# Performance work log

Hardware: AMD Instinct MI355X
Metric: run time of the kernel (lower is better)

The kernel has to match this reference:

```python
import jax, jax.numpy as jnp
import numpy as np

N_NODES = 50000
N_EDGES = 1600000
IN_DIM = 128
HEADS = 8
OUT_C = 16  # per-head channels; HEADS*OUT_C == IN_DIM -> residual active
NEG_SLOPE = 0.2
BN_EPS = 1e-5


def setup_inputs() -> dict:
    key = jax.random.key(0)
    ks = jax.random.split(key, 8)
    x = jax.random.normal(ks[0], (N_NODES, IN_DIM), dtype=jnp.float32)
    edge_index = jax.random.randint(ks[1], (2, N_EDGES), 0, N_NODES, dtype=jnp.int64)
    # GATConv params (PyG: shared lin for src/dst on single-tensor input)
    W = jax.random.normal(ks[2], (IN_DIM, HEADS * OUT_C), dtype=jnp.float32) / np.sqrt(IN_DIM)
    att_src = jax.random.normal(ks[3], (HEADS, OUT_C), dtype=jnp.float32) / np.sqrt(OUT_C)
    att_dst = jax.random.normal(ks[4], (HEADS, OUT_C), dtype=jnp.float32) / np.sqrt(OUT_C)
    bias = jnp.zeros((HEADS * OUT_C,), dtype=jnp.float32)
    # BatchNorm1d affine params
    gamma = jnp.ones((HEADS * OUT_C,), dtype=jnp.float32)
    beta = jnp.zeros((HEADS * OUT_C,), dtype=jnp.float32)
    return {"x": x, "edge_index": edge_index, "W": W, "att_src": att_src,
            "att_dst": att_dst, "bias": bias, "gamma": gamma, "beta": beta}


def reference(x, edge_index, W, att_src, att_dst, bias, gamma, beta):
    N = x.shape[0]
    H, C = att_src.shape
    src, dst = edge_index[0], edge_index[1]

    xl = (x @ W).reshape(N, H, C)                      # [N,H,C]
    a_src = jnp.sum(xl * att_src[None], axis=-1)       # [N,H]
    a_dst = jnp.sum(xl * att_dst[None], axis=-1)       # [N,H]

    e = jax.nn.leaky_relu(a_src[src] + a_dst[dst], NEG_SLOPE)  # [E,H]
    # segment softmax over incoming edges of each dst node
    m = jax.ops.segment_max(e, dst, num_segments=N)    # [N,H], -inf for empty
    m = jnp.where(jnp.isfinite(m), m, 0.0)
    ex = jnp.exp(e - m[dst])                           # [E,H]
    denom = jax.ops.segment_sum(ex, dst, num_segments=N)
    alpha = ex / (denom[dst] + 1e-16)                  # [E,H]

    out = jax.ops.segment_sum(alpha[:, :, None] * xl[src], dst, num_segments=N)  # [N,H,C]
    h = out.reshape(N, H * C) + bias

    # BatchNorm1d (training mode: batch statistics, biased variance)
    mean = jnp.mean(h, axis=0)
    var = jnp.mean((h - mean) ** 2, axis=0)
    h = (h - mean) * jax.lax.rsqrt(var + BN_EPS) * gamma + beta

    h = jax.nn.relu(h)
    return x + h  # residual (in_dim == H*C)
```

## Files before the change

### kernel.cpp

```cpp
#include <hip/hip_runtime.h>
#include <hip/hip_fp16.h>
#include <math.h>

#define N_NODES 50000
#define N_EDGES 1600000
#define DIM 128
#define HEADS 8
#define NEG_SLOPE 0.2f
#define BN_EPS 1e-5f

typedef _Float16 f16x8 __attribute__((ext_vector_type(8)));
typedef float f32x4 __attribute__((ext_vector_type(4)));

__global__ void k_wprep(const float* __restrict__ W, __half* __restrict__ Wh,
                        int* __restrict__ bcur, float* __restrict__ gsums) {
    const int t = threadIdx.x;
    if (blockIdx.x == 0 && t < 256) bcur[t] = 0;
    if (blockIdx.x == 1 && t < 256) gsums[t] = 0.f;
    const int tid = blockIdx.x * 256 + t;
    const int g = tid >> 6;
    const int lane = tid & 63;
    const int nt = g >> 2, kt = g & 3;
    const int q = lane >> 4, n = lane & 15;
    #pragma unroll
    for (int j = 0; j < 8; ++j)
        Wh[(size_t)(g * 64 + lane) * 8 + j] =
            __float2half(W[(kt * 32 + q * 8 + j) * DIM + nt * 16 + n]);
}

__global__ __launch_bounds__(256) void k_lin(const float* __restrict__ x,
                      const __half* __restrict__ Wh, const float* __restrict__ att_s,
                      const float* __restrict__ att_d, __half* __restrict__ xlh,
                      float* __restrict__ a_src, float* __restrict__ a_dst) {
    const int wave = threadIdx.x >> 6;
    const int lane = threadIdx.x & 63;
    const int q = lane >> 4, n = lane & 15;
    const int nb = (blockIdx.x * 4 + wave) * 16;

    const int rowA = min(nb + n, N_NODES - 1);
    const float* xr = x + (size_t)rowA * DIM;
    f16x8 a[4];
    #pragma unroll
    for (int kt = 0; kt < 4; ++kt) {
        const float4 p0 = *(const float4*)(xr + kt * 32 + q * 8);
        const float4 p1 = *(const float4*)(xr + kt * 32 + q * 8 + 4);
        a[kt][0] = (_Float16)p0.x; a[kt][1] = (_Float16)p0.y;
        a[kt][2] = (_Float16)p0.z; a[kt][3] = (_Float16)p0.w;
        a[kt][4] = (_Float16)p1.x; a[kt][5] = (_Float16)p1.y;
        a[kt][6] = (_Float16)p1.z; a[kt][7] = (_Float16)p1.w;
    }

    f32x4 acc[8];
    #pragma unroll
    for (int nt = 0; nt < 8; ++nt) acc[nt] = (f32x4){0.f, 0.f, 0.f, 0.f};

    const f16x8* wb = (const f16x8*)Wh;
    #pragma unroll
    for (int nt = 0; nt < 8; ++nt) {
        #pragma unroll
        for (int kt = 0; kt < 4; ++kt) {
            const f16x8 b = wb[(nt * 4 + kt) * 64 + lane];
            acc[nt] = __builtin_amdgcn_mfma_f32_16x16x32_f16(a[kt], b, acc[nt], 0, 0, 0);
        }
    }

    const int r0 = nb + q * 4;
    #pragma unroll
    for (int nt = 0; nt < 8; ++nt) {
        const float as = att_s[nt * 16 + n];
        const float ad = att_d[nt * 16 + n];
        #pragma unroll
        for (int r = 0; r < 4; ++r) {
            const int row = r0 + r;
            const float v = acc[nt][r];
            float s = v * as;
            float d = v * ad;
            #pragma unroll
            for (int off = 8; off; off >>= 1) {
                s += __shfl_xor(s, off, 16);
                d += __shfl_xor(d, off, 16);
            }
            if (row < N_NODES) {
                xlh[(size_t)row * DIM + nt * 16 + n] = __float2half(v);
                if (n == 0) {
                    a_src[row * HEADS + nt] = s;
                    a_dst[row * HEADS + nt] = d;
                }
            }
        }
    }
}

#define NBUCK 196
#define SEGCAP 12288
#define CHUNK 8192
#define NB_A ((N_EDGES + CHUNK - 1) / CHUNK)

__global__ __launch_bounds__(1024) void k_binA(const int* __restrict__ ei,
                                               int* __restrict__ bcur,
                                               unsigned int* __restrict__ pairs) {
    __shared__ int hist[NBUCK], excl[NBUCK], gbase[NBUCK], cnt2[NBUCK];
    __shared__ int sc[256];
    __shared__ unsigned int buf[CHUNK];
    const int t = threadIdx.x;
    const int base = blockIdx.x * CHUNK;
    const int cnt = min(CHUNK, N_EDGES - base);

    for (int j = t; j < NBUCK; j += 1024) { hist[j] = 0; cnt2[j] = 0; }
    __syncthreads();
    for (int i = t * 4; i < cnt; i += 4096) {
        const int4 dv = *(const int4*)(ei + N_EDGES + base + i);
        atomicAdd(&hist[dv.x >> 8], 1);
        atomicAdd(&hist[dv.y >> 8], 1);
        atomicAdd(&hist[dv.z >> 8], 1);
        atomicAdd(&hist[dv.w >> 8], 1);
    }
    __syncthreads();
    if (t < 256) sc[t] = (t < NBUCK) ? hist[t] : 0;
    __syncthreads();
    for (int d = 1; d < 256; d <<= 1) {
        int xo = 0;
        if (t < 256 && t >= d) xo = sc[t - d];
        __syncthreads();
        if (t < 256) sc[t] += xo;
        __syncthreads();
    }
    if (t < NBUCK) {
        excl[t] = sc[t] - hist[t];
        gbase[t] = t * SEGCAP + atomicAdd(&bcur[t], hist[t]);
    }
    __syncthreads();
    for (int i = t * 4; i < cnt; i += 4096) {
        const int4 sv = *(const int4*)(ei + base + i);
        const int4 dv = *(const int4*)(ei + N_EDGES + base + i);
        const int ss[4] = {sv.x, sv.y, sv.z, sv.w};
        const int dd[4] = {dv.x, dv.y, dv.z, dv.w};
        #pragma unroll
        for (int k = 0; k < 4; ++k) {
            const int b = dd[k] >> 8;
            const int r = atomicAdd(&cnt2[b], 1);
            buf[excl[b] + r] = (unsigned int)ss[k] | ((unsigned int)(dd[k] & 255) << 16)
                             | ((unsigned int)b << 24);
        }
    }
    __syncthreads();
    for (int i = t; i < cnt; i += 1024) {
        const unsigned int u = buf[i];
        const int b = u >> 24;
        pairs[gbase[b] + (i - excl[b])] = u & 0xFFFFFF;
    }
}

__global__ __launch_bounds__(1024) void k_binB(const unsigned int* __restrict__ pairs,
                                               const int* __restrict__ bcur,
                                               unsigned short* __restrict__ csr,
                                               int2* __restrict__ nrange) {
    __shared__ int hist[256], eh[256], excl[256], cnt2[256];
    __shared__ int plen;
    __shared__ unsigned short out[SEGCAP];
    const int t = threadIdx.x;
    const int b = blockIdx.x;
    const int lo = b * SEGCAP;
    const int cnt = bcur[b];

    if (t < 256) { hist[t] = 0; cnt2[t] = 0; }
    __syncthreads();
    for (int i = t; i < cnt; i += 1024)
        atomicAdd(&hist[pairs[lo + i] >> 16], 1);
    __syncthreads();
    if (t < 256) { eh[t] = (hist[t] + 1) & ~1; excl[t] = eh[t]; }
    __syncthreads();
    for (int d = 1; d < 256; d <<= 1) {
        int xo = 0;
        if (t < 256 && t >= d) xo = excl[t - d];
        __syncthreads();
        if (t < 256) excl[t] += xo;
        __syncthreads();
    }
    if (t < 256) excl[t] -= eh[t];
    if (t == 255) plen = excl[255] + eh[255];
    __syncthreads();
    for (int i = t; i < cnt; i += 1024) {
        const unsigned int u = pairs[lo + i];
        const int dl = u >> 16;
        const int r = atomicAdd(&cnt2[dl], 1);
        out[excl[dl] + r] = (unsigned short)(u & 0xFFFF);
    }
    __syncthreads();
    const int pl = plen;
    for (int i = t; i < pl; i += 1024)
        csr[2 * lo + i] = out[i];
    if (t < 256) {
        const int node = (b << 8) + t;
        if (node < N_NODES) {
            int2 rg;
            rg.x = 2 * lo + excl[t];
            rg.y = rg.x + hist[t];
            nrange[node] = rg;
        }
    }
}

#define AGG_NB (N_NODES / 4)

__global__ void k_aggr6(const int2* __restrict__ nrange,
                        const unsigned short* __restrict__ csr,
                        const float* __restrict__ a_src, const float* __restrict__ a_dst,
                        const __half* __restrict__ xlh, float* __restrict__ y) {
    const int d = blockIdx.x * 4 + (threadIdx.x >> 6);
    const int lane = threadIdx.x & 63;
    const int c2 = lane << 1;
    const int h = lane >> 3;
    const int2 rg = nrange[d];
    const int lo = rg.x, hi = rg.y;
    const float ad = a_dst[d * HEADS + h];
    float acc0 = 0.f, acc1 = 0.f, dsum = 0.f;
    int i = lo;
    for (; i + 8 <= hi; i += 8) {
        int s[8];
        float e[8];
        __half2 xv[8];
        #pragma unroll
        for (int j = 0; j < 8; ++j) s[j] = csr[i + j];
        #pragma unroll
        for (int j = 0; j < 8; ++j) e[j] = a_src[s[j] * HEADS + h] + ad;
        #pragma unroll
        for (int j = 0; j < 8; ++j)
            xv[j] = *(const __half2*)(xlh + (size_t)s[j] * DIM + c2);
        #pragma unroll
        for (int j = 0; j < 8; ++j) {
            const float w = __expf(fmaxf(e[j], NEG_SLOPE * e[j]));
            const float2 f = __half22float2(xv[j]);
            acc0 = fmaf(w, f.x, acc0);
            acc1 = fmaf(w, f.y, acc1);
            dsum += w;
        }
    }
    for (; i < hi; ++i) {
        const int s = csr[i];
        const float e = a_src[s * HEADS + h] + ad;
        const __half2 xv = *(const __half2*)(xlh + (size_t)s * DIM + c2);
        const float w = __expf(fmaxf(e, NEG_SLOPE * e));
        const float2 f = __half22float2(xv);
        acc0 = fmaf(w, f.x, acc0); acc1 = fmaf(w, f.y, acc1); dsum += w;
    }
    const float inv = 1.f / (dsum + 1e-16f);
    float2 o; o.x = acc0 * inv; o.y = acc1 * inv;
    *(float2*)(y + (size_t)d * DIM + c2) = o;
}

__global__ void k_stats(const float* __restrict__ y, const float* __restrict__ bias,
                        float* __restrict__ gsums) {
    const int c = threadIdx.x;
    const float b = bias[c];
    float s = 0.f, ss = 0.f;
    for (int n = blockIdx.x; n < N_NODES; n += gridDim.x) {
        const float h = y[n * DIM + c] + b;
        s += h;
        ss += h * h;
    }
    atomicAdd(&gsums[c], s);
    atomicAdd(&gsums[DIM + c], ss);
}

__global__ void k_final(float* __restrict__ y, const float* __restrict__ x,
                        const float* __restrict__ sums, const float* __restrict__ sumsq,
                        const float* __restrict__ gamma, const float* __restrict__ beta,
                        const float* __restrict__ bias) {
    const int q = blockIdx.x * blockDim.x + threadIdx.x;
    const int cq = q & (DIM / 4 - 1);
    const float4 sm = ((const float4*)sums)[cq];
    const float4 sq = ((const float4*)sumsq)[cq];
    const float4 gm = ((const float4*)gamma)[cq];
    const float4 bt = ((const float4*)beta)[cq];
    const float4 bs = ((const float4*)bias)[cq];
    float4 v = ((const float4*)y)[q];
    const float4 xv = ((const float4*)x)[q];
    const float inv_n = 1.f / (float)N_NODES;
#define BNC(c) { const float mean = sm.c * inv_n;                         \
                 const float var = sq.c * inv_n - mean * mean;            \
                 const float sc = rsqrtf(var + BN_EPS) * gm.c;            \
                 const float sh = bt.c + (bs.c - mean) * sc;              \
                 v.c = xv.c + fmaxf(v.c * sc + sh, 0.f); }
    BNC(x) BNC(y) BNC(z) BNC(w)
#undef BNC
    ((float4*)y)[q] = v;
}

extern "C" void kernel_launch(void* const* d_in, const int* in_sizes, int n_in,
                              void* d_out, int out_size, void* d_ws, size_t ws_size,
                              hipStream_t stream) {
    const float* x     = (const float*)d_in[0];
    const int*   ei    = (const int*)  d_in[1];
    const float* W     = (const float*)d_in[2];
    const float* att_s = (const float*)d_in[3];
    const float* att_d = (const float*)d_in[4];
    const float* bias  = (const float*)d_in[5];
    const float* gamma = (const float*)d_in[6];
    const float* beta  = (const float*)d_in[7];
    float* y = (float*)d_out;

    __half* xlh  = (__half*)d_ws;
    float* a_src = (float*)(xlh + (size_t)N_NODES * DIM);
    float* a_dst = a_src + (size_t)N_NODES * HEADS;
    float* sums  = a_dst + (size_t)N_NODES * HEADS;
    float* sumsq = sums  + DIM;
    int*   bcur  = (int*)(sumsq + DIM);
    int2*  nrange = (int2*)(bcur + 256);
    __half* Wh   = (__half*)(nrange + N_NODES);
    unsigned int* pairs = (unsigned int*)(Wh + 16384);
    unsigned short* csr = (unsigned short*)pairs;

    k_wprep<<<8, 256, 0, stream>>>(W, Wh, bcur, sums);
    k_lin<<<(N_NODES + 63) / 64, 256, 0, stream>>>(x, Wh, att_s, att_d, xlh, a_src, a_dst);
    k_binA<<<NB_A, 1024, 0, stream>>>(ei, bcur, pairs);
    k_binB<<<NBUCK, 1024, 0, stream>>>(pairs, bcur, csr, nrange);
    k_aggr6<<<AGG_NB, 256, 0, stream>>>(nrange, csr, a_src, a_dst, xlh, y);
    k_stats<<<512, DIM, 0, stream>>>(y, bias, sums);
    k_final<<<(size_t)N_NODES * DIM / 4 / 256, 256, 0, stream>>>(y, x, sums, sumsq,
                                                                 gamma, beta, bias);
}
```

Measured before the change: 239.7 us.

## Fuse linear projection and edge binning into one heterogeneous kernel launch

```diff
diff --git a/kernel.cpp b/kernel.cpp
--- a/kernel.cpp
+++ b/kernel.cpp
@@ -12,154 +12,159 @@
 typedef _Float16 f16x8 __attribute__((ext_vector_type(8)));
 typedef float f32x4 __attribute__((ext_vector_type(4)));
 
-__global__ void k_wprep(const float* __restrict__ W, __half* __restrict__ Wh,
-                        int* __restrict__ bcur, float* __restrict__ gsums) {
-    const int t = threadIdx.x;
-    if (blockIdx.x == 0 && t < 256) bcur[t] = 0;
-    if (blockIdx.x == 1 && t < 256) gsums[t] = 0.f;
-    const int tid = blockIdx.x * 256 + t;
-    const int g = tid >> 6;
-    const int lane = tid & 63;
-    const int nt = g >> 2, kt = g & 3;
-    const int q = lane >> 4, n = lane & 15;
-    #pragma unroll
-    for (int j = 0; j < 8; ++j)
-        Wh[(size_t)(g * 64 + lane) * 8 + j] =
-            __float2half(W[(kt * 32 + q * 8 + j) * DIM + nt * 16 + n]);
-}
-
-__global__ __launch_bounds__(256) void k_lin(const float* __restrict__ x,
-                      const __half* __restrict__ Wh, const float* __restrict__ att_s,
-                      const float* __restrict__ att_d, __half* __restrict__ xlh,
-                      float* __restrict__ a_src, float* __restrict__ a_dst) {
-    const int wave = threadIdx.x >> 6;
-    const int lane = threadIdx.x & 63;
-    const int q = lane >> 4, n = lane & 15;
-    const int nb = (blockIdx.x * 4 + wave) * 16;
-
-    const int rowA = min(nb + n, N_NODES - 1);
-    const float* xr = x + (size_t)rowA * DIM;
-    f16x8 a[4];
-    #pragma unroll
-    for (int kt = 0; kt < 4; ++kt) {
-        const float4 p0 = *(const float4*)(xr + kt * 32 + q * 8);
-        const float4 p1 = *(const float4*)(xr + kt * 32 + q * 8 + 4);
-        a[kt][0] = (_Float16)p0.x; a[kt][1] = (_Float16)p0.y;
-        a[kt][2] = (_Float16)p0.z; a[kt][3] = (_Float16)p0.w;
-        a[kt][4] = (_Float16)p1.x; a[kt][5] = (_Float16)p1.y;
-        a[kt][6] = (_Float16)p1.z; a[kt][7] = (_Float16)p1.w;
-    }
-
-    f32x4 acc[8];
-    #pragma unroll
-    for (int nt = 0; nt < 8; ++nt) acc[nt] = (f32x4){0.f, 0.f, 0.f, 0.f};
-
-    const f16x8* wb = (const f16x8*)Wh;
-    #pragma unroll
-    for (int nt = 0; nt < 8; ++nt) {
-        #pragma unroll
-        for (int kt = 0; kt < 4; ++kt) {
-            const f16x8 b = wb[(nt * 4 + kt) * 64 + lane];
-            acc[nt] = __builtin_amdgcn_mfma_f32_16x16x32_f16(a[kt], b, acc[nt], 0, 0, 0);
-        }
-    }
-
-    const int r0 = nb + q * 4;
-    #pragma unroll
-    for (int nt = 0; nt < 8; ++nt) {
-        const float as = att_s[nt * 16 + n];
-        const float ad = att_d[nt * 16 + n];
-        #pragma unroll
-        for (int r = 0; r < 4; ++r) {
-            const int row = r0 + r;
-            const float v = acc[nt][r];
-            float s = v * as;
-            float d = v * ad;
-            #pragma unroll
-            for (int off = 8; off; off >>= 1) {
-                s += __shfl_xor(s, off, 16);
-                d += __shfl_xor(d, off, 16);
-            }
-            if (row < N_NODES) {
-                xlh[(size_t)row * DIM + nt * 16 + n] = __float2half(v);
-                if (n == 0) {
-                    a_src[row * HEADS + nt] = s;
-                    a_dst[row * HEADS + nt] = d;
-                }
-            }
-        }
-    }
-}
-
 #define NBUCK 196
 #define SEGCAP 12288
 #define CHUNK 8192
 #define NB_A ((N_EDGES + CHUNK - 1) / CHUNK)
-
-__global__ __launch_bounds__(1024) void k_binA(const int* __restrict__ ei,
-                                               int* __restrict__ bcur,
-                                               unsigned int* __restrict__ pairs) {
-    __shared__ int hist[NBUCK], excl[NBUCK], gbase[NBUCK], cnt2[NBUCK];
-    __shared__ int sc[256];
-    __shared__ unsigned int buf[CHUNK];
+#define LIN_NB ((N_NODES + 127) / 128)
+#define FUSED_NB (NB_A + LIN_NB)
+
+struct BinAShm {
+    int hist[NBUCK], excl[NBUCK], gbase[NBUCK], cnt2[NBUCK];
+    int sc[256];
+    unsigned int buf[CHUNK];
+};
+struct LinShm { __half wh[16384]; };
+
+__global__ __launch_bounds__(512) void k_linbinA(
+        const float* __restrict__ x, const float* __restrict__ W,
+        const float* __restrict__ att_s, const float* __restrict__ att_d,
+        const int* __restrict__ ei, int* __restrict__ bcur,
+        unsigned int* __restrict__ pairs, __half* __restrict__ xlh,
+        float* __restrict__ a_src, float* __restrict__ a_dst) {
+    __shared__ union { BinAShm a; LinShm l; } sh;
     const int t = threadIdx.x;
-    const int base = blockIdx.x * CHUNK;
-    const int cnt = min(CHUNK, N_EDGES - base);
-
-    for (int j = t; j < NBUCK; j += 1024) { hist[j] = 0; cnt2[j] = 0; }
-    __syncthreads();
-    for (int i = t * 4; i < cnt; i += 4096) {
-        const int4 dv = *(const int4*)(ei + N_EDGES + base + i);
-        atomicAdd(&hist[dv.x >> 8], 1);
-        atomicAdd(&hist[dv.y >> 8], 1);
-        atomicAdd(&hist[dv.z >> 8], 1);
-        atomicAdd(&hist[dv.w >> 8], 1);
-    }
-    __syncthreads();
-    if (t < 256) sc[t] = (t < NBUCK) ? hist[t] : 0;
-    __syncthreads();
-    for (int d = 1; d < 256; d <<= 1) {
-        int xo = 0;
-        if (t < 256 && t >= d) xo = sc[t - d];
-        __syncthreads();
-        if (t < 256) sc[t] += xo;
-        __syncthreads();
-    }
-    if (t < NBUCK) {
-        excl[t] = sc[t] - hist[t];
-        gbase[t] = t * SEGCAP + atomicAdd(&bcur[t], hist[t]);
-    }
-    __syncthreads();
-    for (int i = t * 4; i < cnt; i += 4096) {
-        const int4 sv = *(const int4*)(ei + base + i);
-        const int4 dv = *(const int4*)(ei + N_EDGES + base + i);
-        const int ss[4] = {sv.x, sv.y, sv.z, sv.w};
-        const int dd[4] = {dv.x, dv.y, dv.z, dv.w};
-        #pragma unroll
-        for (int k = 0; k < 4; ++k) {
-            const int b = dd[k] >> 8;
-            const int r = atomicAdd(&cnt2[b], 1);
-            buf[excl[b] + r] = (unsigned int)ss[k] | ((unsigned int)(dd[k] & 255) << 16)
-                             | ((unsigned int)b << 24);
-        }
-    }
-    __syncthreads();
-    for (int i = t; i < cnt; i += 1024) {
-        const unsigned int u = buf[i];
-        const int b = u >> 24;
-        pairs[gbase[b] + (i - excl[b])] = u & 0xFFFFFF;
+
+    if (blockIdx.x < NB_A) {
+        const int base = blockIdx.x * CHUNK;
+        const int cnt = min(CHUNK, N_EDGES - base);
+
+        for (int j = t; j < NBUCK; j += 512) { sh.a.hist[j] = 0; sh.a.cnt2[j] = 0; }
+        __syncthreads();
+        for (int i = t * 4; i < cnt; i += 2048) {
+            const int4 dv = *(const int4*)(ei + N_EDGES + base + i);
+            atomicAdd(&sh.a.hist[dv.x >> 8], 1);
+            atomicAdd(&sh.a.hist[dv.y >> 8], 1);
+            atomicAdd(&sh.a.hist[dv.z >> 8], 1);
+            atomicAdd(&sh.a.hist[dv.w >> 8], 1);
+        }
+        __syncthreads();
+        if (t < 256) sh.a.sc[t] = (t < NBUCK) ? sh.a.hist[t] : 0;
+        __syncthreads();
+        for (int d = 1; d < 256; d <<= 1) {
+            int xo = 0;
+            if (t < 256 && t >= d) xo = sh.a.sc[t - d];
+            __syncthreads();
+            if (t < 256) sh.a.sc[t] += xo;
+            __syncthreads();
+        }
+        if (t < NBUCK) {
+            sh.a.excl[t] = sh.a.sc[t] - sh.a.hist[t];
+            sh.a.gbase[t] = t * SEGCAP + atomicAdd(&bcur[t], sh.a.hist[t]);
+        }
+        __syncthreads();
+        for (int i = t * 4; i < cnt; i += 2048) {
+            const int4 sv = *(const int4*)(ei + base + i);
+            const int4 dv = *(const int4*)(ei + N_EDGES + base + i);
+            const int ss[4] = {sv.x, sv.y, sv.z, sv.w};
+            const int dd[4] = {dv.x, dv.y, dv.z, dv.w};
+            #pragma unroll
+            for (int k = 0; k < 4; ++k) {
+                const int b = dd[k] >> 8;
+                const int r = atomicAdd(&sh.a.cnt2[b], 1);
+                sh.a.buf[sh.a.excl[b] + r] = (unsigned int)ss[k]
+                    | ((unsigned int)(dd[k] & 255) << 16) | ((unsigned int)b << 24);
+            }
+        }
+        __syncthreads();
+        for (int i = t; i < cnt; i += 512) {
+            const unsigned int u = sh.a.buf[i];
+            const int b = u >> 24;
+            pairs[sh.a.gbase[b] + (i - sh.a.excl[b])] = u & 0xFFFFFF;
+        }
+    } else {
+        for (int v = t; v < 2048; v += 512) {
+            const int g = v >> 6, lane = v & 63;
+            const int nt = g >> 2, kt = g & 3;
+            const int q = lane >> 4, n = lane & 15;
+            #pragma unroll
+            for (int j = 0; j < 8; ++j)
+                sh.l.wh[(size_t)(g * 64 + lane) * 8 + j] =
+                    __float2half(W[(kt * 32 + q * 8 + j) * DIM + nt * 16 + n]);
+        }
+        __syncthreads();
+
+        const int wave = t >> 6;
+        const int lane = t & 63;
+        const int q = lane >> 4, n = lane & 15;
+        const int nb = ((blockIdx.x - NB_A) * 8 + wave) * 16;
+
+        const int rowA = min(nb + n, N_NODES - 1);
+        const float* xr = x + (size_t)rowA * DIM;
+        f16x8 a[4];
+        #pragma unroll
+        for (int kt = 0; kt < 4; ++kt) {
+            const float4 p0 = *(const float4*)(xr + kt * 32 + q * 8);
+            const float4 p1 = *(const float4*)(xr + kt * 32 + q * 8 + 4);
+            a[kt][0] = (_Float16)p0.x; a[kt][1] = (_Float16)p0.y;
+            a[kt][2] = (_Float16)p0.z; a[kt][3] = (_Float16)p0.w;
+            a[kt][4] = (_Float16)p1.x; a[kt][5] = (_Float16)p1.y;
+            a[kt][6] = (_Float16)p1.z; a[kt][7] = (_Float16)p1.w;
+        }
+
+        f32x4 acc[8];
+        #pragma unroll
+        for (int nt = 0; nt < 8; ++nt) acc[nt] = (f32x4){0.f, 0.f, 0.f, 0.f};
+
+        const f16x8* wb = (const f16x8*)sh.l.wh;
+        #pragma unroll
+        for (int nt = 0; nt < 8; ++nt) {
+            #pragma unroll
+            for (int kt = 0; kt < 4; ++kt) {
+                const f16x8 b = wb[(nt * 4 + kt) * 64 + lane];
+                acc[nt] = __builtin_amdgcn_mfma_f32_16x16x32_f16(a[kt], b, acc[nt], 0, 0, 0);
+            }
+        }
+
+        const int r0 = nb + q * 4;
+        #pragma unroll
+        for (int nt = 0; nt < 8; ++nt) {
+            const float as = att_s[nt * 16 + n];
+            const float ad = att_d[nt * 16 + n];
+            #pragma unroll
+            for (int r = 0; r < 4; ++r) {
+                const int row = r0 + r;
+                const float v = acc[nt][r];
+                float s = v * as;
+                float d = v * ad;
+                #pragma unroll
+                for (int off = 8; off; off >>= 1) {
+                    s += __shfl_xor(s, off, 16);
+                    d += __shfl_xor(d, off, 16);
+                }
+                if (row < N_NODES) {
+                    xlh[(size_t)row * DIM + nt * 16 + n] = __float2half(v);
+                    if (n == 0) {
+                        a_src[row * HEADS + nt] = s;
+                        a_dst[row * HEADS + nt] = d;
+                    }
+                }
+            }
+        }
     }
 }
 
 __global__ __launch_bounds__(1024) void k_binB(const unsigned int* __restrict__ pairs,
                                                const int* __restrict__ bcur,
                                                unsigned short* __restrict__ csr,
-                                               int2* __restrict__ nrange) {
+                                               int2* __restrict__ nrange,
+                                               float* __restrict__ gsums) {
     __shared__ int hist[256], eh[256], excl[256], cnt2[256];
     __shared__ int plen;
     __shared__ unsigned short out[SEGCAP];
     const int t = threadIdx.x;
     const int b = blockIdx.x;
+    if (b == 0 && t < 256) gsums[t] = 0.f;
     const int lo = b * SEGCAP;
     const int cnt = bcur[b];
 
@@ -307,14 +312,13 @@
     float* sumsq = sums  + DIM;
     int*   bcur  = (int*)(sumsq + DIM);
     int2*  nrange = (int2*)(bcur + 256);
-    __half* Wh   = (__half*)(nrange + N_NODES);
-    unsigned int* pairs = (unsigned int*)(Wh + 16384);
+    unsigned int* pairs = (unsigned int*)(nrange + N_NODES);
     unsigned short* csr = (unsigned short*)pairs;
 
-    k_wprep<<<8, 256, 0, stream>>>(W, Wh, bcur, sums);
-    k_lin<<<(N_NODES + 63) / 64, 256, 0, stream>>>(x, Wh, att_s, att_d, xlh, a_src, a_dst);
-    k_binA<<<NB_A, 1024, 0, stream>>>(ei, bcur, pairs);
-    k_binB<<<NBUCK, 1024, 0, stream>>>(pairs, bcur, csr, nrange);
+    hipMemsetAsync(bcur, 0, 256 * sizeof(int), stream);
+    k_linbinA<<<FUSED_NB, 512, 0, stream>>>(x, W, att_s, att_d, ei, bcur, pairs,
+                                            xlh, a_src, a_dst);
+    k_binB<<<NBUCK, 1024, 0, stream>>>(pairs, bcur, csr, nrange, sums);
     k_aggr6<<<AGG_NB, 256, 0, stream>>>(nrange, csr, a_src, a_dst, xlh, y);
     k_stats<<<512, DIM, 0, stream>>>(y, bias, sums);
     k_final<<<(size_t)N_NODES * DIM / 4 / 256, 256, 0, stream>>>(y, x, sums, sumsq,
```

Result: faster. 233.2 us (-2.7%).
